# Performance work log

Measured on AMD Instinct MI355X. Metric: run time of the kernel, lower is better.

The kernel has to match this reference:

```python
import jax, jax.numpy as jnp
import numpy as np

HEADS = 4
DIM_HEAD = 32
SCALE = DIM_HEAD ** -0.5
GN_EPS = 1e-5


def setup_inputs() -> dict:
    key = jax.random.key(0)
    k1, k2, k3 = jax.random.split(key, 3)
    dim, hidden = 64, HEADS * DIM_HEAD
    x = jax.random.normal(k1, (2, dim, 32, 32, 32), dtype=jnp.float32)
    w_qkv = jax.random.normal(k2, (3 * hidden, dim), dtype=jnp.float32) * (dim ** -0.5)
    w_out = jax.random.normal(k3, (dim, hidden), dtype=jnp.float32) * (hidden ** -0.5)
    b_out = jnp.zeros((dim,), dtype=jnp.float32)
    gn_w = jnp.ones((dim,), dtype=jnp.float32)
    gn_b = jnp.zeros((dim,), dtype=jnp.float32)
    return {"x": x, "w_qkv": w_qkv, "w_out": w_out, "b_out": b_out, "gn_w": gn_w, "gn_b": gn_b}


def reference(x, w_qkv, w_out, b_out, gn_w, gn_b):
    b, c, D, H, W = x.shape
    n = D * H * W
    xf = x.reshape(b, c, n)  # flatten spatial: 1x1 Conv3d == channel matmul
    qkv = jnp.einsum('oc,bcn->bon', w_qkv, xf)  # [b, 3*hidden, n]
    q, k, v = jnp.split(qkv, 3, axis=1)
    rs = lambda t: t.reshape(b, HEADS, DIM_HEAD, n)  # b h d n
    q, k, v = rs(q), rs(k), rs(v)
    q = jax.nn.softmax(q, axis=2) * SCALE   # softmax over head-dim channels
    k = jax.nn.softmax(k, axis=3)           # softmax over spatial positions
    context = jnp.einsum('bhdn,bhen->bhde', k, v)   # [b, h, d, e], tiny
    out = jnp.einsum('bhde,bhdn->bhen', context, q)  # [b, h, e, n]
    out = out.reshape(b, HEADS * DIM_HEAD, n)
    # to_out: 1x1 Conv3d with bias, then GroupNorm(1, dim)
    y = jnp.einsum('oc,bcn->bon', w_out, out) + b_out[None, :, None]
    mean = jnp.mean(y, axis=(1, 2), keepdims=True)
    var = jnp.var(y, axis=(1, 2), keepdims=True)
    y = (y - mean) * jax.lax.rsqrt(var + GN_EPS)
    y = y * gn_w[None, :, None] + gn_b[None, :, None]
    return y.reshape(b, -1, D, H, W)
```

## Files before the change

kernel.cpp:

```cpp
#include <hip/hip_runtime.h>
#include <hip/hip_bf16.h>

#define NB 2
#define C_IN 64
#define N_SP 32768
#define NHEADS 4
#define DH 32
#define HID 128
#define QK_SCALE 0.17677669529663687f
#define GN_EPS_C 1e-5f
#define NGN 2097152.0f

using bf16x8 = __attribute__((ext_vector_type(8))) short;
using f32x4  = __attribute__((ext_vector_type(4))) float;
using u16x4  = __attribute__((ext_vector_type(4))) unsigned short;
using u16x8  = __attribute__((ext_vector_type(8))) unsigned short;

__device__ __forceinline__ unsigned short f2bf(float f) {
    union { float f; unsigned u; } c{f};
    unsigned r = c.u + 0x7FFFu + ((c.u >> 16) & 1u);
    return (unsigned short)(r >> 16);
}
__device__ __forceinline__ float bf2f(unsigned short u) {
    union { unsigned u; float f; } c{ (unsigned)u << 16 };
    return c.f;
}

__device__ __forceinline__ void load_xf(const float* __restrict__ xb, int n0,
        int lg, int lc, bf16x8 xf[2][2]) {
#pragma unroll
    for (int s = 0; s < 2; ++s) {
        int n = n0 + s * 16 + lc;
#pragma unroll
        for (int kk = 0; kk < 2; ++kk) {
            bf16x8 v;
#pragma unroll
            for (int j = 0; j < 8; ++j)
                v[j] = (short)f2bf(xb[(size_t)(kk * 32 + lg * 8 + j) * N_SP + n]);
            xf[s][kk] = v;
        }
    }
}

__global__ __launch_bounds__(256) void kprep(const float* __restrict__ wqkv,
        unsigned short* __restrict__ wfrag) {
    int t = threadIdx.x;
#pragma unroll
    for (int i = 0; i < 12; ++i) {
        int idx = t + i * 256;
        int f = idx >> 6, lane = idx & 63;
        int mt = f >> 1, kk = f & 1;
        int row = mt * 16 + (lane & 15);
        int c0 = kk * 32 + (lane >> 4) * 8;
        const float* wp = wqkv + row * 64 + c0;
        unsigned short* op = wfrag + (size_t)idx * 8;
#pragma unroll
        for (int j = 0; j < 8; ++j) op[j] = f2bf(wp[j]);
    }
}

__global__ __launch_bounds__(512) void kA(const float* __restrict__ x,
        const unsigned short* __restrict__ wfrag,
        float* __restrict__ ctx_part, float* __restrict__ ksum_part) {
    __shared__ unsigned short kt[8192];
    __shared__ unsigned short vt[8192];
    const int t = threadIdx.x, wv = t >> 6, l = t & 63, lg = l >> 4, lc = l & 15;
    const int blk = blockIdx.x;
    const int b = blk >> 7, nblk = blk & 127;
    const int n0 = nblk * 256 + wv * 32;

    bf16x8 xf[2][2];
    load_xf(x + (size_t)b * C_IN * N_SP, n0, lg, lc, xf);

    const int di = (wv >> 1) & 1, ei = wv & 1;
#pragma unroll
    for (int h = 0; h < NHEADS; ++h) {
        f32x4 ka[2][2] = {}, va[2][2] = {};
#pragma unroll
        for (int e = 0; e < 2; ++e)
#pragma unroll
            for (int kk = 0; kk < 2; ++kk) {
                bf16x8 wk = *(const bf16x8*)(wfrag + ((size_t)((8 + 2 * h + e) * 2 + kk) * 64 + l) * 8);
                bf16x8 wf = *(const bf16x8*)(wfrag + ((size_t)((16 + 2 * h + e) * 2 + kk) * 64 + l) * 8);
#pragma unroll
                for (int s = 0; s < 2; ++s) {
                    ka[s][e] = __builtin_amdgcn_mfma_f32_16x16x32_bf16(xf[s][kk], wk, ka[s][e], 0, 0, 0);
                    va[s][e] = __builtin_amdgcn_mfma_f32_16x16x32_bf16(xf[s][kk], wf, va[s][e], 0, 0, 0);
                }
            }
        __syncthreads();
#pragma unroll
        for (int s = 0; s < 2; ++s)
#pragma unroll
            for (int e = 0; e < 2; ++e) {
                u16x4 pk, pv;
#pragma unroll
                for (int r = 0; r < 4; ++r) {
                    pk[r] = f2bf(__expf(ka[s][e][r]));
                    pv[r] = f2bf(va[s][e][r]);
                }
                int ch = e * 16 + lc;
                int pos = wv * 32 + s * 16 + lg * 4;
                int ba = (ch * 512 + pos * 2) ^ ((ch & 7) << 4);
                *(u16x4*)((char*)kt + ba) = pk;
                *(u16x4*)((char*)vt + ba) = pv;
            }
        __syncthreads();
        if (wv < 4) {
            f32x4 ca = {};
            float ks = 0.f;
#pragma unroll
            for (int k0 = 0; k0 < 256; k0 += 32) {
                int ar = di * 16 + lc, br = ei * 16 + lc;
                bf16x8 af = *(const bf16x8*)((const char*)kt + ((ar * 512 + (k0 + lg * 8) * 2) ^ ((ar & 7) << 4)));
                bf16x8 bf = *(const bf16x8*)((const char*)vt + ((br * 512 + (k0 + lg * 8) * 2) ^ ((br & 7) << 4)));
                if (ei == 0) {
#pragma unroll
                    for (int j = 0; j < 8; ++j) ks += bf2f((unsigned short)af[j]);
                }
                ca = __builtin_amdgcn_mfma_f32_16x16x32_bf16(af, bf, ca, 0, 0, 0);
            }
            float* cp = ctx_part + ((size_t)(b * 4 + h) * 128 + nblk) * 1024;
#pragma unroll
            for (int r = 0; r < 4; ++r)
                cp[(di * 16 + lg * 4 + r) * 32 + ei * 16 + lc] = ca[r];
            if (ei == 0) {
                ks += __shfl_xor(ks, 16);
                ks += __shfl_xor(ks, 32);
                if (lg == 0)
                    ksum_part[((size_t)(b * 4 + h) * 128 + nblk) * 32 + di * 16 + lc] = ks;
            }
        }
    }
}

__global__ __launch_bounds__(256) void kB(const float* __restrict__ ctx_part,
        const float* __restrict__ ksum_part, const float* __restrict__ wout,
        unsigned short* __restrict__ weff) {
    __shared__ float cred2[2][128];
    __shared__ float cred[128];
    __shared__ float ks2[4][32];
    __shared__ float ksl[4];
    const int blk = blockIdx.x;
    const int g = blk >> 3, ds = blk & 7;
    const int bb = g >> 2, h = g & 3;
    const int t = threadIdx.x;
    const int tt = t & 127, th = t >> 7;
    float a = 0.f;
    const float* cp = ctx_part + ((size_t)g * 128 + th * 64) * 1024 + ds * 128 + tt;
#pragma unroll 8
    for (int i = 0; i < 64; ++i) a += cp[(size_t)i * 1024];
    cred2[th][tt] = a;
    if (t < 128) {
        int dl = t >> 5, ic = t & 31;
        float s = 0.f;
        const float* kp = ksum_part + ((size_t)g * 128 + ic * 4) * 32 + ds * 4 + dl;
#pragma unroll
        for (int i = 0; i < 4; ++i) s += kp[i * 32];
        ks2[dl][ic] = s;
    }
    __syncthreads();
    if (t < 128) cred[t] = cred2[0][t] + cred2[1][t];
    if (t < 4) {
        float s = 0.f;
#pragma unroll
        for (int i = 0; i < 32; ++i) s += ks2[t][i];
        ksl[t] = s;
    }
    __syncthreads();
    const int o = t >> 2, dl = t & 3;
    const float* wrow = wout + o * HID + h * 32;
    const float* crow = cred + dl * 32;
    float acc = 0.f;
#pragma unroll
    for (int e = 0; e < 32; ++e) acc = fmaf(wrow[e], crow[e], acc);
    acc /= ksl[dl];
    weff[((size_t)bb * 64 + o) * 128 + h * 32 + ds * 4 + dl] = f2bf(acc);
}

__global__ __launch_bounds__(512) void kC(const float* __restrict__ x,
        const unsigned short* __restrict__ wfrag, const unsigned short* __restrict__ weff,
        const float* __restrict__ bout, unsigned short* __restrict__ y_t,
        float* __restrict__ pstats) {
    __shared__ unsigned short qt[256 * 128];
    __shared__ float red[16];
    const int t = threadIdx.x, wv = t >> 6, l = t & 63, lg = l >> 4, lc = l & 15;
    const int blk = blockIdx.x;
    const int b = blk >> 7, nblk = blk & 127;
    const int n0 = nblk * 256 + wv * 32;

    bf16x8 xf[2][2];
    load_xf(x + (size_t)b * C_IN * N_SP, n0, lg, lc, xf);

#pragma unroll
    for (int h = 0; h < NHEADS; ++h) {
        f32x4 qa[2][2] = {};
#pragma unroll
        for (int mi = 0; mi < 2; ++mi)
#pragma unroll
            for (int kk = 0; kk < 2; ++kk) {
                bf16x8 aq = *(const bf16x8*)(wfrag + ((size_t)((h * 2 + mi) * 2 + kk) * 64 + l) * 8);
#pragma unroll
                for (int s = 0; s < 2; ++s)
                    qa[mi][s] = __builtin_amdgcn_mfma_f32_16x16x32_bf16(aq, xf[s][kk], qa[mi][s], 0, 0, 0);
            }
#pragma unroll
        for (int s = 0; s < 2; ++s) {
            float m = -1e30f;
#pragma unroll
            for (int mi = 0; mi < 2; ++mi)
#pragma unroll
                for (int r = 0; r < 4; ++r) m = fmaxf(m, qa[mi][s][r]);
            m = fmaxf(m, __shfl_xor(m, 16));
            m = fmaxf(m, __shfl_xor(m, 32));
            float sum = 0.f;
#pragma unroll
            for (int mi = 0; mi < 2; ++mi)
#pragma unroll
                for (int r = 0; r < 4; ++r) {
                    float e = __expf(qa[mi][s][r] - m);
                    qa[mi][s][r] = e; sum += e;
                }
            sum += __shfl_xor(sum, 16);
            sum += __shfl_xor(sum, 32);
            float inv = QK_SCALE / sum;
            int pos = wv * 32 + s * 16 + lc;
            int swz = (pos & 7) << 4;
#pragma unroll
            for (int mi = 0; mi < 2; ++mi) {
                u16x4 pk;
#pragma unroll
                for (int r = 0; r < 4; ++r) pk[r] = f2bf(qa[mi][s][r] * inv);
                int ch0 = h * 32 + mi * 16 + lg * 4;
                *(u16x4*)((char*)qt + ((pos * 256 + ch0 * 2) ^ swz)) = pk;
            }
        }
    }

    f32x4 acc[4][2] = {};
    const unsigned short* wb = weff + (size_t)b * 8192;
#pragma unroll
    for (int kk = 0; kk < 4; ++kk) {
        bf16x8 bq[2];
#pragma unroll
        for (int s = 0; s < 2; ++s) {
            int pos = wv * 32 + s * 16 + lc;
            bq[s] = *(const bf16x8*)((const char*)qt +
                ((pos * 256 + (kk * 32 + lg * 8) * 2) ^ ((pos & 7) << 4)));
        }
#pragma unroll
        for (int mt = 0; mt < 4; ++mt) {
            bf16x8 af = *(const bf16x8*)(wb + (size_t)(mt * 16 + lc) * 128 + kk * 32 + lg * 8);
#pragma unroll
            for (int s = 0; s < 2; ++s)
                acc[mt][s] = __builtin_amdgcn_mfma_f32_16x16x32_bf16(af, bq[s], acc[mt][s], 0, 0, 0);
        }
    }
    float s1 = 0.f, s2 = 0.f;
#pragma unroll
    for (int mt = 0; mt < 4; ++mt) {
        float bo[4];
#pragma unroll
        for (int r = 0; r < 4; ++r) bo[r] = bout[mt * 16 + lg * 4 + r];
#pragma unroll
        for (int s = 0; s < 2; ++s) {
            u16x4 pk;
#pragma unroll
            for (int r = 0; r < 4; ++r) {
                float val = acc[mt][s][r] + bo[r];
                s1 += val;
                s2 = fmaf(val, val, s2);
                pk[r] = f2bf(val);
            }
            int n = n0 + s * 16 + lc;
            *(u16x4*)(y_t + ((size_t)b * N_SP + n) * 64 + mt * 16 + lg * 4) = pk;
        }
    }
#pragma unroll
    for (int off = 32; off > 0; off >>= 1) {
        s1 += __shfl_down(s1, off, 64);
        s2 += __shfl_down(s2, off, 64);
    }
    if (l == 0) { red[wv * 2] = s1; red[wv * 2 + 1] = s2; }
    __syncthreads();
    if (t == 0) {
        float S1 = 0.f, S2 = 0.f;
#pragma unroll
        for (int w = 0; w < 8; ++w) { S1 += red[w * 2]; S2 += red[w * 2 + 1]; }
        pstats[(b * 128 + nblk) * 2]     = S1;
        pstats[(b * 128 + nblk) * 2 + 1] = S2;
    }
}

__global__ __launch_bounds__(256) void kE(const unsigned short* __restrict__ y_t,
        const float* __restrict__ pstats, const float* __restrict__ gnw,
        const float* __restrict__ gnb, float* __restrict__ out) {
    __shared__ float red[4];
    __shared__ float ms[2];
    __shared__ float w2s[64], b2s[64];
    const int t = threadIdx.x;
    const int blk = blockIdx.x;
    const int b = blk >> 9, nb = blk & 511;
    float s1 = 0.f, s2 = 0.f;
    if (t < 128) {
        s1 = pstats[(b * 128 + t) * 2];
        s2 = pstats[(b * 128 + t) * 2 + 1];
    }
#pragma unroll
    for (int off = 32; off > 0; off >>= 1) {
        s1 += __shfl_down(s1, off, 64);
        s2 += __shfl_down(s2, off, 64);
    }
    if (t < 128 && (t & 63) == 0) { red[(t >> 6) * 2] = s1; red[(t >> 6) * 2 + 1] = s2; }
    __syncthreads();
    if (t == 0) {
        float S1 = red[0] + red[2], S2 = red[1] + red[3];
        float mean = S1 / NGN;
        float var = S2 / NGN - mean * mean;
        ms[0] = mean; ms[1] = rsqrtf(var + GN_EPS_C);
    }
    __syncthreads();
    if (t < 64) {
        float w2 = gnw[t] * ms[1];
        w2s[t] = w2;
        b2s[t] = gnb[t] - ms[0] * w2;
    }
    __syncthreads();
    const int n = nb * 64 + (t & 63), o0 = (t >> 6) * 16;
    const unsigned short* yp = y_t + ((size_t)b * N_SP + n) * 64 + o0;
    u16x8 v0 = *(const u16x8*)yp;
    u16x8 v1 = *(const u16x8*)(yp + 8);
    float* ob = out + (size_t)b * C_IN * N_SP + n;
#pragma unroll
    for (int j = 0; j < 8; ++j)
        ob[(size_t)(o0 + j) * N_SP] = fmaf(bf2f((unsigned short)v0[j]), w2s[o0 + j], b2s[o0 + j]);
#pragma unroll
    for (int j = 0; j < 8; ++j)
        ob[(size_t)(o0 + 8 + j) * N_SP] = fmaf(bf2f((unsigned short)v1[j]), w2s[o0 + 8 + j], b2s[o0 + 8 + j]);
}

extern "C" void kernel_launch(void* const* d_in, const int* in_sizes, int n_in,
                              void* d_out, int out_size, void* d_ws, size_t ws_size,
                              hipStream_t stream) {
    const float* x    = (const float*)d_in[0];
    const float* wqkv = (const float*)d_in[1];
    const float* wout = (const float*)d_in[2];
    const float* bout = (const float*)d_in[3];
    const float* gnw  = (const float*)d_in[4];
    const float* gnb  = (const float*)d_in[5];
    float* out = (float*)d_out;

    char* ws = (char*)d_ws;
    size_t off = 0;
    unsigned short* wfrag = (unsigned short*)(ws + off); off += 49152;
    float* ctx_part  = (float*)(ws + off); off += (size_t)8 * 128 * 1024 * 4;
    float* ksum_part = (float*)(ws + off); off += (size_t)8 * 128 * 32 * 4;
    unsigned short* weff = (unsigned short*)(ws + off); off += 2 * 8192 * 2;
    unsigned short* y_t  = (unsigned short*)(ws + off); off += (size_t)NB * N_SP * 64 * 2;
    float* pstats = (float*)(ws + off); off += NB * 128 * 2 * 4;

    kprep<<<dim3(1), dim3(256), 0, stream>>>(wqkv, wfrag);
    kA<<<dim3(256), dim3(512), 0, stream>>>(x, wfrag, ctx_part, ksum_part);
    kB<<<dim3(64), dim3(256), 0, stream>>>(ctx_part, ksum_part, wout, weff);
    kC<<<dim3(256), dim3(512), 0, stream>>>(x, wfrag, weff, bout, y_t, pstats);
    kE<<<dim3(1024), dim3(256), 0, stream>>>(y_t, pstats, gnw, gnb, out);
}
```

Baseline: 47.30 us.

## Pre-transpose x to bf16 channel-last buffer and double-buffer kA shared tiles

Adds a kernel that converts x once into a bf16 position-major layout (and folds the weight-fragment prep into it), so kA and kC load their MFMA operands as contiguous 16-byte vectors instead of strided scalar fp32 gathers done twice. kA also double-buffers its K/V shared-memory tiles by head parity, removing one barrier per head. The cost is an extra 8 MB write plus reread through global memory and a larger shared-memory footprint in kA.

Measured after the change: 47.24 us. About the same (-0.1%).

```diff
diff --git a/kernel.cpp b/kernel.cpp
--- a/kernel.cpp
+++ b/kernel.cpp
@@ -26,55 +26,61 @@
     return c.f;
 }
 
-__device__ __forceinline__ void load_xf(const float* __restrict__ xb, int n0,
-        int lg, int lc, bf16x8 xf[2][2]) {
-#pragma unroll
-    for (int s = 0; s < 2; ++s) {
-        int n = n0 + s * 16 + lc;
-#pragma unroll
-        for (int kk = 0; kk < 2; ++kk) {
-            bf16x8 v;
-#pragma unroll
-            for (int j = 0; j < 8; ++j)
-                v[j] = (short)f2bf(xb[(size_t)(kk * 32 + lg * 8 + j) * N_SP + n]);
-            xf[s][kk] = v;
-        }
-    }
-}
-
-__global__ __launch_bounds__(256) void kprep(const float* __restrict__ wqkv,
+__global__ __launch_bounds__(128) void kXW(const float* __restrict__ x,
+        const float* __restrict__ wqkv, unsigned short* __restrict__ x_t,
         unsigned short* __restrict__ wfrag) {
-    int t = threadIdx.x;
-#pragma unroll
-    for (int i = 0; i < 12; ++i) {
-        int idx = t + i * 256;
-        int f = idx >> 6, lane = idx & 63;
-        int mt = f >> 1, kk = f & 1;
-        int row = mt * 16 + (lane & 15);
-        int c0 = kk * 32 + (lane >> 4) * 8;
-        const float* wp = wqkv + row * 64 + c0;
-        unsigned short* op = wfrag + (size_t)idx * 8;
-#pragma unroll
-        for (int j = 0; j < 8; ++j) op[j] = f2bf(wp[j]);
-    }
-}
-
-__global__ __launch_bounds__(512) void kA(const float* __restrict__ x,
+    const int blk = blockIdx.x, t = threadIdx.x;
+    if (blk == 512) {
+#pragma unroll
+        for (int i = 0; i < 24; ++i) {
+            int idx = t + i * 128;
+            int f = idx >> 6, lane = idx & 63;
+            int mt = f >> 1, kk = f & 1;
+            int row = mt * 16 + (lane & 15);
+            int c0 = kk * 32 + (lane >> 4) * 8;
+            const float* wp = wqkv + row * 64 + c0;
+            unsigned short* op = wfrag + (size_t)idx * 8;
+#pragma unroll
+            for (int j = 0; j < 8; ++j) op[j] = f2bf(wp[j]);
+        }
+        return;
+    }
+    const int b = blk >> 8;
+    const int n = (blk & 255) * 128 + t;
+    const float* xb = x + (size_t)b * C_IN * N_SP + n;
+    unsigned short* op = x_t + ((size_t)b * N_SP + n) * 64;
+#pragma unroll
+    for (int c8 = 0; c8 < 8; ++c8) {
+        u16x8 pk;
+#pragma unroll
+        for (int j = 0; j < 8; ++j)
+            pk[j] = f2bf(xb[(size_t)(c8 * 8 + j) * N_SP]);
+        *(u16x8*)(op + c8 * 8) = pk;
+    }
+}
+
+__global__ __launch_bounds__(512) void kA(const unsigned short* __restrict__ x_t,
         const unsigned short* __restrict__ wfrag,
         float* __restrict__ ctx_part, float* __restrict__ ksum_part) {
-    __shared__ unsigned short kt[8192];
-    __shared__ unsigned short vt[8192];
+    __shared__ unsigned short kt[2][8192];
+    __shared__ unsigned short vt[2][8192];
     const int t = threadIdx.x, wv = t >> 6, l = t & 63, lg = l >> 4, lc = l & 15;
     const int blk = blockIdx.x;
     const int b = blk >> 7, nblk = blk & 127;
     const int n0 = nblk * 256 + wv * 32;
 
     bf16x8 xf[2][2];
-    load_xf(x + (size_t)b * C_IN * N_SP, n0, lg, lc, xf);
+#pragma unroll
+    for (int s = 0; s < 2; ++s)
+#pragma unroll
+        for (int kk = 0; kk < 2; ++kk)
+            xf[s][kk] = *(const bf16x8*)(x_t +
+                ((size_t)b * N_SP + n0 + s * 16 + lc) * 64 + kk * 32 + lg * 8);
 
     const int di = (wv >> 1) & 1, ei = wv & 1;
 #pragma unroll
     for (int h = 0; h < NHEADS; ++h) {
+        const int bs = h & 1;
         f32x4 ka[2][2] = {}, va[2][2] = {};
 #pragma unroll
         for (int e = 0; e < 2; ++e)
@@ -88,7 +94,6 @@
                     va[s][e] = __builtin_amdgcn_mfma_f32_16x16x32_bf16(xf[s][kk], wf, va[s][e], 0, 0, 0);
                 }
             }
-        __syncthreads();
 #pragma unroll
         for (int s = 0; s < 2; ++s)
 #pragma unroll
@@ -102,8 +107,8 @@
                 int ch = e * 16 + lc;
                 int pos = wv * 32 + s * 16 + lg * 4;
                 int ba = (ch * 512 + pos * 2) ^ ((ch & 7) << 4);
-                *(u16x4*)((char*)kt + ba) = pk;
-                *(u16x4*)((char*)vt + ba) = pv;
+                *(u16x4*)((char*)kt[bs] + ba) = pk;
+                *(u16x4*)((char*)vt[bs] + ba) = pv;
             }
         __syncthreads();
         if (wv < 4) {
@@ -112,8 +117,8 @@
 #pragma unroll
             for (int k0 = 0; k0 < 256; k0 += 32) {
                 int ar = di * 16 + lc, br = ei * 16 + lc;
-                bf16x8 af = *(const bf16x8*)((const char*)kt + ((ar * 512 + (k0 + lg * 8) * 2) ^ ((ar & 7) << 4)));
-                bf16x8 bf = *(const bf16x8*)((const char*)vt + ((br * 512 + (k0 + lg * 8) * 2) ^ ((br & 7) << 4)));
+                bf16x8 af = *(const bf16x8*)((const char*)kt[bs] + ((ar * 512 + (k0 + lg * 8) * 2) ^ ((ar & 7) << 4)));
+                bf16x8 bf = *(const bf16x8*)((const char*)vt[bs] + ((br * 512 + (k0 + lg * 8) * 2) ^ ((br & 7) << 4)));
                 if (ei == 0) {
 #pragma unroll
                     for (int j = 0; j < 8; ++j) ks += bf2f((unsigned short)af[j]);
@@ -178,7 +183,7 @@
     weff[((size_t)bb * 64 + o) * 128 + h * 32 + ds * 4 + dl] = f2bf(acc);
 }
 
-__global__ __launch_bounds__(512) void kC(const float* __restrict__ x,
+__global__ __launch_bounds__(512) void kC(const unsigned short* __restrict__ x_t,
         const unsigned short* __restrict__ wfrag, const unsigned short* __restrict__ weff,
         const float* __restrict__ bout, unsigned short* __restrict__ y_t,
         float* __restrict__ pstats) {
@@ -190,7 +195,12 @@
     const int n0 = nblk * 256 + wv * 32;
 
     bf16x8 xf[2][2];
-    load_xf(x + (size_t)b * C_IN * N_SP, n0, lg, lc, xf);
+#pragma unroll
+    for (int s = 0; s < 2; ++s)
+#pragma unroll
+        for (int kk = 0; kk < 2; ++kk)
+            xf[s][kk] = *(const bf16x8*)(x_t +
+                ((size_t)b * N_SP + n0 + s * 16 + lc) * 64 + kk * 32 + lg * 8);
 
 #pragma unroll
     for (int h = 0; h < NHEADS; ++h) {
@@ -353,15 +363,16 @@
     char* ws = (char*)d_ws;
     size_t off = 0;
     unsigned short* wfrag = (unsigned short*)(ws + off); off += 49152;
+    unsigned short* x_t   = (unsigned short*)(ws + off); off += (size_t)NB * N_SP * 64 * 2;
     float* ctx_part  = (float*)(ws + off); off += (size_t)8 * 128 * 1024 * 4;
     float* ksum_part = (float*)(ws + off); off += (size_t)8 * 128 * 32 * 4;
     unsigned short* weff = (unsigned short*)(ws + off); off += 2 * 8192 * 2;
     unsigned short* y_t  = (unsigned short*)(ws + off); off += (size_t)NB * N_SP * 64 * 2;
     float* pstats = (float*)(ws + off); off += NB * 128 * 2 * 4;
 
-    kprep<<<dim3(1), dim3(256), 0, stream>>>(wqkv, wfrag);
-    kA<<<dim3(256), dim3(512), 0, stream>>>(x, wfrag, ctx_part, ksum_part);
+    kXW<<<dim3(513), dim3(128), 0, stream>>>(x, wqkv, x_t, wfrag);
+    kA<<<dim3(256), dim3(512), 0, stream>>>(x_t, wfrag, ctx_part, ksum_part);
     kB<<<dim3(64), dim3(256), 0, stream>>>(ctx_part, ksum_part, wout, weff);
-    kC<<<dim3(256), dim3(512), 0, stream>>>(x, wfrag, weff, bout, y_t, pstats);
+    kC<<<dim3(256), dim3(512), 0, stream>>>(x_t, wfrag, weff, bout, y_t, pstats);
     kE<<<dim3(1024), dim3(256), 0, stream>>>(y_t, pstats, gnw, gnb, out);
 }
```

## Fuse weight bf16 packing into kA/kC and double-buffer K/V tiles

Applied to the files above, without the earlier changes.

Removes the single-block kprep kernel and its launch. Each block of kA and kC now converts its own slice of w_qkv to bf16 MFMA fragments in shared memory, then reads the weights from LDS instead of global memory. kA also double-buffers the K/V staging tiles by head parity, which drops one __syncthreads per head. The cost is redundant weight conversion in every block and more LDS per block, which may reduce occupancy.

Result: faster. 42.93 us (-9.2%).

```diff
diff --git a/kernel.cpp b/kernel.cpp
--- a/kernel.cpp
+++ b/kernel.cpp
@@ -42,53 +42,51 @@
     }
 }
 
-__global__ __launch_bounds__(256) void kprep(const float* __restrict__ wqkv,
-        unsigned short* __restrict__ wfrag) {
-    int t = threadIdx.x;
-#pragma unroll
-    for (int i = 0; i < 12; ++i) {
-        int idx = t + i * 256;
-        int f = idx >> 6, lane = idx & 63;
-        int mt = f >> 1, kk = f & 1;
-        int row = mt * 16 + (lane & 15);
-        int c0 = kk * 32 + (lane >> 4) * 8;
-        const float* wp = wqkv + row * 64 + c0;
-        unsigned short* op = wfrag + (size_t)idx * 8;
-#pragma unroll
-        for (int j = 0; j < 8; ++j) op[j] = f2bf(wp[j]);
-    }
-}
-
 __global__ __launch_bounds__(512) void kA(const float* __restrict__ x,
-        const unsigned short* __restrict__ wfrag,
+        const float* __restrict__ wqkv,
         float* __restrict__ ctx_part, float* __restrict__ ksum_part) {
-    __shared__ unsigned short kt[8192];
-    __shared__ unsigned short vt[8192];
+    __shared__ unsigned short wl[32 * 64 * 8];
+    __shared__ unsigned short kt[2][8192];
+    __shared__ unsigned short vt[2][8192];
     const int t = threadIdx.x, wv = t >> 6, l = t & 63, lg = l >> 4, lc = l & 15;
     const int blk = blockIdx.x;
     const int b = blk >> 7, nblk = blk & 127;
     const int n0 = nblk * 256 + wv * 32;
 
+#pragma unroll
+    for (int i = 0; i < 4; ++i) {
+        int idx = t + i * 512;
+        int f = idx >> 6, lane = idx & 63;
+        int row = (8 + (f >> 1)) * 16 + (lane & 15);
+        int c0 = (f & 1) * 32 + (lane >> 4) * 8;
+        const float* wp = wqkv + row * 64 + c0;
+        u16x8 pk;
+#pragma unroll
+        for (int j = 0; j < 8; ++j) pk[j] = f2bf(wp[j]);
+        *(u16x8*)(wl + (size_t)idx * 8) = pk;
+    }
+
     bf16x8 xf[2][2];
     load_xf(x + (size_t)b * C_IN * N_SP, n0, lg, lc, xf);
+    __syncthreads();
 
     const int di = (wv >> 1) & 1, ei = wv & 1;
 #pragma unroll
     for (int h = 0; h < NHEADS; ++h) {
+        const int bs = h & 1;
         f32x4 ka[2][2] = {}, va[2][2] = {};
 #pragma unroll
         for (int e = 0; e < 2; ++e)
 #pragma unroll
             for (int kk = 0; kk < 2; ++kk) {
-                bf16x8 wk = *(const bf16x8*)(wfrag + ((size_t)((8 + 2 * h + e) * 2 + kk) * 64 + l) * 8);
-                bf16x8 wf = *(const bf16x8*)(wfrag + ((size_t)((16 + 2 * h + e) * 2 + kk) * 64 + l) * 8);
+                bf16x8 wk = *(const bf16x8*)(wl + ((size_t)((2 * h + e) * 2 + kk) * 64 + l) * 8);
+                bf16x8 wf = *(const bf16x8*)(wl + ((size_t)(16 + (2 * h + e) * 2 + kk) * 64 + l) * 8);
 #pragma unroll
                 for (int s = 0; s < 2; ++s) {
                     ka[s][e] = __builtin_amdgcn_mfma_f32_16x16x32_bf16(xf[s][kk], wk, ka[s][e], 0, 0, 0);
                     va[s][e] = __builtin_amdgcn_mfma_f32_16x16x32_bf16(xf[s][kk], wf, va[s][e], 0, 0, 0);
                 }
             }
-        __syncthreads();
 #pragma unroll
         for (int s = 0; s < 2; ++s)
 #pragma unroll
@@ -102,8 +100,8 @@
                 int ch = e * 16 + lc;
                 int pos = wv * 32 + s * 16 + lg * 4;
                 int ba = (ch * 512 + pos * 2) ^ ((ch & 7) << 4);
-                *(u16x4*)((char*)kt + ba) = pk;
-                *(u16x4*)((char*)vt + ba) = pv;
+                *(u16x4*)((char*)kt[bs] + ba) = pk;
+                *(u16x4*)((char*)vt[bs] + ba) = pv;
             }
         __syncthreads();
         if (wv < 4) {
@@ -112,8 +110,8 @@
 #pragma unroll
             for (int k0 = 0; k0 < 256; k0 += 32) {
                 int ar = di * 16 + lc, br = ei * 16 + lc;
-                bf16x8 af = *(const bf16x8*)((const char*)kt + ((ar * 512 + (k0 + lg * 8) * 2) ^ ((ar & 7) << 4)));
-                bf16x8 bf = *(const bf16x8*)((const char*)vt + ((br * 512 + (k0 + lg * 8) * 2) ^ ((br & 7) << 4)));
+                bf16x8 af = *(const bf16x8*)((const char*)kt[bs] + ((ar * 512 + (k0 + lg * 8) * 2) ^ ((ar & 7) << 4)));
+                bf16x8 bf = *(const bf16x8*)((const char*)vt[bs] + ((br * 512 + (k0 + lg * 8) * 2) ^ ((br & 7) << 4)));
                 if (ei == 0) {
 #pragma unroll
                     for (int j = 0; j < 8; ++j) ks += bf2f((unsigned short)af[j]);
@@ -179,9 +177,10 @@
 }
 
 __global__ __launch_bounds__(512) void kC(const float* __restrict__ x,
-        const unsigned short* __restrict__ wfrag, const unsigned short* __restrict__ weff,
+        const float* __restrict__ wqkv, const unsigned short* __restrict__ weff,
         const float* __restrict__ bout, unsigned short* __restrict__ y_t,
         float* __restrict__ pstats) {
+    __shared__ unsigned short wl[16 * 64 * 8];
     __shared__ unsigned short qt[256 * 128];
     __shared__ float red[16];
     const int t = threadIdx.x, wv = t >> 6, l = t & 63, lg = l >> 4, lc = l & 15;
@@ -189,8 +188,22 @@
     const int b = blk >> 7, nblk = blk & 127;
     const int n0 = nblk * 256 + wv * 32;
 
+#pragma unroll
+    for (int i = 0; i < 2; ++i) {
+        int idx = t + i * 512;
+        int f = idx >> 6, lane = idx & 63;
+        int row = (f >> 1) * 16 + (lane & 15);
+        int c0 = (f & 1) * 32 + (lane >> 4) * 8;
+        const float* wp = wqkv + row * 64 + c0;
+        u16x8 pk;
+#pragma unroll
+        for (int j = 0; j < 8; ++j) pk[j] = f2bf(wp[j]);
+        *(u16x8*)(wl + (size_t)idx * 8) = pk;
+    }
+
     bf16x8 xf[2][2];
     load_xf(x + (size_t)b * C_IN * N_SP, n0, lg, lc, xf);
+    __syncthreads();
 
 #pragma unroll
     for (int h = 0; h < NHEADS; ++h) {
@@ -199,7 +212,7 @@
         for (int mi = 0; mi < 2; ++mi)
 #pragma unroll
             for (int kk = 0; kk < 2; ++kk) {
-                bf16x8 aq = *(const bf16x8*)(wfrag + ((size_t)((h * 2 + mi) * 2 + kk) * 64 + l) * 8);
+                bf16x8 aq = *(const bf16x8*)(wl + ((size_t)((h * 2 + mi) * 2 + kk) * 64 + l) * 8);
 #pragma unroll
                 for (int s = 0; s < 2; ++s)
                     qa[mi][s] = __builtin_amdgcn_mfma_f32_16x16x32_bf16(aq, xf[s][kk], qa[mi][s], 0, 0, 0);
@@ -352,16 +365,14 @@
 
     char* ws = (char*)d_ws;
     size_t off = 0;
-    unsigned short* wfrag = (unsigned short*)(ws + off); off += 49152;
     float* ctx_part  = (float*)(ws + off); off += (size_t)8 * 128 * 1024 * 4;
     float* ksum_part = (float*)(ws + off); off += (size_t)8 * 128 * 32 * 4;
     unsigned short* weff = (unsigned short*)(ws + off); off += 2 * 8192 * 2;
     unsigned short* y_t  = (unsigned short*)(ws + off); off += (size_t)NB * N_SP * 64 * 2;
     float* pstats = (float*)(ws + off); off += NB * 128 * 2 * 4;
 
-    kprep<<<dim3(1), dim3(256), 0, stream>>>(wqkv, wfrag);
-    kA<<<dim3(256), dim3(512), 0, stream>>>(x, wfrag, ctx_part, ksum_part);
+    kA<<<dim3(256), dim3(512), 0, stream>>>(x, wqkv, ctx_part, ksum_part);
     kB<<<dim3(64), dim3(256), 0, stream>>>(ctx_part, ksum_part, wout, weff);
-    kC<<<dim3(256), dim3(512), 0, stream>>>(x, wfrag, weff, bout, y_t, pstats);
+    kC<<<dim3(256), dim3(512), 0, stream>>>(x, wqkv, weff, bout, y_t, pstats);
     kE<<<dim3(1024), dim3(256), 0, stream>>>(y_t, pstats, gnw, gnb, out);
 }
```
